# Performance work log

Hardware: AMD Instinct MI355X
Metric: run time of the kernel (lower is better)

## Reference

```python
import jax, jax.numpy as jnp
import numpy as np

N = 10000        # nodes
E = 320000       # edges (before self-loops)
G = 100          # graphs in batch
HEADS = 2
OUT = 125        # per-head out channels
NEG_SLOPE = 0.2  # PyG GATConv default leaky_relu slope


def setup_inputs() -> dict:
    key = jax.random.key(0)
    k = lambda i: jax.random.fold_in(key, i)
    rn = lambda i, shape, s=0.1: jax.random.normal(k(i), shape, jnp.float32) * s
    inp = {
        "x": jax.random.normal(k(0), (N, 336), jnp.float32),
        "edge_index": jax.random.randint(k(1), (2, E), 0, N, jnp.int32),
        "batch": jnp.sort(jax.random.randint(k(2), (N,), 0, G, jnp.int32)),
    }
    conv_in = [336, 250, 250, 250]
    for i, din in enumerate(conv_in, start=1):
        base = 10 * i
        inp[f"W{i}"] = rn(base, (din, HEADS * OUT))
        inp[f"asrc{i}"] = rn(base + 1, (HEADS, OUT))
        inp[f"adst{i}"] = rn(base + 2, (HEADS, OUT))
        inp[f"b{i}"] = jnp.zeros((HEADS * OUT,), jnp.float32)
    lin_dims = [(250, 200), (200, 100), (100, 100), (100, 29)]
    for i, (din, dout) in enumerate(lin_dims, start=1):
        inp[f"lw{i}"] = rn(100 + i, (din, dout))
        inp[f"lb{i}"] = jnp.zeros((dout,), jnp.float32)
    return inp


def gat_conv(x, src, dst, W, asrc, adst, b):
    # PyG GATConv (v1), concat heads, self-loops already in (src, dst).
    n = x.shape[0]
    h = (x @ W).reshape(n, HEADS, OUT)                    # [N,H,C]
    e_src = jnp.einsum('nhc,hc->nh', h, asrc)             # a_src . h_j
    e_dst = jnp.einsum('nhc,hc->nh', h, adst)             # a_dst . h_i
    e = jax.nn.leaky_relu(e_src[src] + e_dst[dst], NEG_SLOPE)  # [Etot,H]
    m = jax.ops.segment_max(e, dst, num_segments=n)       # segment softmax over incoming edges
    e = jnp.exp(e - m[dst])
    denom = jax.ops.segment_sum(e, dst, num_segments=n)
    alpha = e / (denom[dst] + 1e-16)                      # [Etot,H]
    out = jax.ops.segment_sum(alpha[:, :, None] * h[src], dst, num_segments=n)
    return out.reshape(n, HEADS * OUT) + b


def reference(x, edge_index, batch,
              W1, asrc1, adst1, b1, W2, asrc2, adst2, b2,
              W3, asrc3, adst3, b3, W4, asrc4, adst4, b4,
              lw1, lb1, lw2, lb2, lw3, lb3, lw4, lb4):
    n = x.shape[0]
    loop = jnp.arange(n, dtype=edge_index.dtype)
    src = jnp.concatenate([edge_index[0], loop])          # add_self_loops=True
    dst = jnp.concatenate([edge_index[1], loop])

    h = jax.nn.relu(gat_conv(x, src, dst, W1, asrc1, adst1, b1))
    h = jax.nn.relu(gat_conv(h, src, dst, W2, asrc2, adst2, b2))
    h = jax.nn.relu(gat_conv(h, src, dst, W3, asrc3, adst3, b3))
    h = jax.nn.relu(gat_conv(h, src, dst, W4, asrc4, adst4, b4))

    # global_mean_pool over graph ids
    sums = jax.ops.segment_sum(h, batch, num_segments=G)
    cnts = jax.ops.segment_sum(jnp.ones((n, 1), h.dtype), batch, num_segments=G)
    g = sums / jnp.maximum(cnts, 1.0)                     # [G,250]

    g = jax.nn.relu(g @ lw1 + lb1)
    g = jax.nn.relu(g @ lw2 + lb2)
    g = jax.nn.relu(g @ lw3 + lb3)
    return g @ lw4 + lb4                                  # [G,29]
```

## Files before the change

kernel.cpp:

```cpp
#include <hip/hip_runtime.h>
#include <hip/hip_bf16.h>

#define NNODES 10000
#define NEDGES 320000
#define ETOT   (NEDGES + NNODES)
#define NGRAPH 100
#define CH     250
#define HOUT   125
#define MPAD   10048
#define NTILE  157
#define KP0    352
#define KP1    256
#define HPAD   256
#define ECAP   128
#define DCAPW  128
#define APAD   264

typedef __attribute__((ext_vector_type(8))) short bf16x8;
typedef __attribute__((ext_vector_type(4))) float f32x4;

static __device__ __forceinline__ float bflo(unsigned int u){
  union{ unsigned int i; float f; } v; v.i = u << 16; return v.f;
}
static __device__ __forceinline__ float bfhi(unsigned int u){
  union{ unsigned int i; float f; } v; v.i = u & 0xffff0000u; return v.f;
}
static __device__ __forceinline__ unsigned short f2bfbits(float f){
  __hip_bfloat16 b = __float2bfloat16(f);
  union{ __hip_bfloat16 b; unsigned short s; } v; v.b = b; return v.s;
}

struct Args {
  const float* x; const int* eidx; const int* batch;
  const float *W0,*W1,*W2,*W3;
  __hip_bfloat16 *Abf0, *Wt0, *Wt1, *Wt2, *Wt3;
  int *cursor; unsigned short* bucket; int *gstart;
};

__global__ void k_pre(Args a){
  int gtid = blockIdx.x * blockDim.x + threadIdx.x;
  int gstr = gridDim.x * blockDim.x;
  for (int e = gtid; e < ETOT; e += gstr){
    int dst, src;
    if (e < NEDGES){ src = a.eidx[e]; dst = a.eidx[NEDGES + e]; }
    else           { src = e - NEDGES; dst = src; }
    int pos = atomicAdd(&a.cursor[dst], 1);
    if (pos < ECAP) a.bucket[(size_t)dst * ECAP + pos] = (unsigned short)src;
  }
  for (int n = gtid; n < NNODES; n += gstr){
    int b1 = a.batch[n];
    int b0 = (n == 0) ? -1 : a.batch[n-1];
    for (int b = b0 + 1; b <= b1; ++b) a.gstart[b] = n;
    if (n == NNODES - 1){
      for (int b = b1 + 1; b <= NGRAPH; ++b) a.gstart[b] = NNODES;
    }
  }
  for (int j = gtid; j < NNODES * 84; j += gstr){
    int r = j / 84, c4 = (j - r * 84) * 4;
    float4 v = *(const float4*)(a.x + (size_t)r * 336 + c4);
    ushort4 o;
    o.x = f2bfbits(v.x); o.y = f2bfbits(v.y); o.z = f2bfbits(v.z); o.w = f2bfbits(v.w);
    *(ushort4*)(a.Abf0 + (size_t)r * KP0 + c4) = o;
  }
  const int T0 = 16 * KP0 * 16;
  const int T1 = 16 * KP1 * 16;
  int tot = T0 + 3*T1;
  for (int i = gtid; i < tot; i += gstr){
    const float* W; __hip_bfloat16* Wt; int K, Kp, li;
    if (i < T0)             { W = a.W0; Wt = a.Wt0; K = 336; Kp = KP0; li = i; }
    else if (i < T0 +   T1) { W = a.W1; Wt = a.Wt1; K = CH;  Kp = KP1; li = i - T0; }
    else if (i < T0 + 2*T1) { W = a.W2; Wt = a.Wt2; K = CH;  Kp = KP1; li = i - T0 - T1; }
    else                    { W = a.W3; Wt = a.Wt3; K = CH;  Kp = KP1; li = i - T0 - 2*T1; }
    int KC = Kp >> 5;
    int nt = li / (Kp * 16);
    int rem = li % (Kp * 16);
    int k = rem / 16;
    int n = rem % 16;
    int col = nt * 16 + n;
    float v = (k < K && col < CH) ? W[(size_t)k * CH + col] : 0.f;
    Wt[(((size_t)nt * KC + (k >> 5)) * 16 + n) * 32 + (k & 31)] = __float2bfloat16(v);
  }
}

__global__ __launch_bounds__(256) void k_gemm(
    const __hip_bfloat16* __restrict__ A, const __hip_bfloat16* __restrict__ Wt,
    __hip_bfloat16* __restrict__ Cb, const float* __restrict__ asrc,
    const float* __restrict__ adst, float* __restrict__ esrc, float* __restrict__ edst,
    int Kp){
  int wv = threadIdx.x >> 6, lane = threadIdx.x & 63;
  int n16 = lane & 15, q = lane >> 4;
  int KC = Kp >> 5;
  int rowbase = blockIdx.x * 64 + wv * 16;
  int bn = blockIdx.y * 64;
  int nt0 = bn >> 4;
  const __hip_bfloat16* ap = A  + (size_t)(rowbase + n16) * Kp + q * 8;
  const __hip_bfloat16* bp = Wt + ((size_t)nt0 * KC * 16 + n16) * 32 + q * 8;
  f32x4 ac0 = {0.f,0.f,0.f,0.f}, ac1 = ac0, ac2 = ac0, ac3 = ac0;
  for (int kc = 0; kc < KC; ++kc){
    bf16x8 a  = *(const bf16x8*)(ap + (size_t)kc * 32);
    bf16x8 b0 = *(const bf16x8*)(bp + ((size_t)0 * KC + kc) * 512);
    bf16x8 b1 = *(const bf16x8*)(bp + ((size_t)1 * KC + kc) * 512);
    bf16x8 b2 = *(const bf16x8*)(bp + ((size_t)2 * KC + kc) * 512);
    bf16x8 b3 = *(const bf16x8*)(bp + ((size_t)3 * KC + kc) * 512);
    ac0 = __builtin_amdgcn_mfma_f32_16x16x32_bf16(a, b0, ac0, 0, 0, 0);
    ac1 = __builtin_amdgcn_mfma_f32_16x16x32_bf16(a, b1, ac1, 0, 0, 0);
    ac2 = __builtin_amdgcn_mfma_f32_16x16x32_bf16(a, b2, ac2, 0, 0, 0);
    ac3 = __builtin_amdgcn_mfma_f32_16x16x32_bf16(a, b3, ac3, 0, 0, 0);
  }
  float es0[4] = {}, es1[4] = {}, ed0a[4] = {}, ed1a[4] = {};
  #define SCORE_T(AC, T) { \
    int col = bn + (T)*16 + n16; \
    bool ok = col < CH; \
    float av = ok ? asrc[col] : 0.f; \
    float dv = ok ? adst[col] : 0.f; \
    bool hh = col >= HOUT; \
    float av0 = hh ? 0.f : av, av1 = hh ? av : 0.f; \
    float dv0 = hh ? 0.f : dv, dv1 = hh ? dv : 0.f; \
    _Pragma("unroll") \
    for (int r = 0; r < 4; ++r){ \
      es0[r] += AC[r]*av0; es1[r] += AC[r]*av1; \
      ed0a[r] += AC[r]*dv0; ed1a[r] += AC[r]*dv1; } }
  SCORE_T(ac0, 0) SCORE_T(ac1, 1) SCORE_T(ac2, 2) SCORE_T(ac3, 3)
  #undef SCORE_T
  #pragma unroll
  for (int off = 1; off < 16; off <<= 1){
    #pragma unroll
    for (int r = 0; r < 4; ++r){
      es0[r]  += __shfl_xor(es0[r],  off);
      es1[r]  += __shfl_xor(es1[r],  off);
      ed0a[r] += __shfl_xor(ed0a[r], off);
      ed1a[r] += __shfl_xor(ed1a[r], off);
    }
  }
  if (n16 == 0){
    #pragma unroll
    for (int r = 0; r < 4; ++r){
      int row = rowbase + q*4 + r;
      if (row < NNODES){
        atomicAdd(&esrc[row*2+0], es0[r]);
        atomicAdd(&esrc[row*2+1], es1[r]);
        atomicAdd(&edst[row*2+0], ed0a[r]);
        atomicAdd(&edst[row*2+1], ed1a[r]);
      }
    }
  }
  #pragma unroll
  for (int r = 0; r < 4; ++r){
    int row = rowbase + q * 4 + r;
    if (row >= NNODES) continue;
    int col = bn + n16;
    __hip_bfloat16* cb = Cb + (size_t)row * HPAD + col;
    cb[0]  = __float2bfloat16(col      < CH ? ac0[r] : 0.f);
    cb[16] = __float2bfloat16(col + 16 < CH ? ac1[r] : 0.f);
    cb[32] = __float2bfloat16(col + 32 < CH ? ac2[r] : 0.f);
    cb[48] = __float2bfloat16(col + 48 < CH ? ac3[r] : 0.f);
  }
}

#define GATHER8(SS, SX) \
  for (int it = half; it < deg; it += 16){ \
    uint4 dv[8]; float a0v[8], a1v[8]; \
    _Pragma("unroll") \
    for (int u = 0; u < 8; ++u){ \
      int ii = it + 2*u; \
      bool vld = ii < deg; \
      int jj = vld ? ii : 0; \
      int s = SS[jj]; \
      float2 xv = SX[jj]; \
      a0v[u] = vld ? xv.x : 0.f; \
      a1v[u] = vld ? xv.y : 0.f; \
      dv[u] = *(const uint4*)(hrow + (size_t)s * HPAD); \
    } \
    _Pragma("unroll") \
    for (int u = 0; u < 8; ++u){ \
      float a0 = a0v[u], a1 = a1v[u]; \
      acc[0] += (0 < n0 ? a0 : a1) * bflo(dv[u].x); \
      acc[1] += (1 < n0 ? a0 : a1) * bfhi(dv[u].x); \
      acc[2] += (2 < n0 ? a0 : a1) * bflo(dv[u].y); \
      acc[3] += (3 < n0 ? a0 : a1) * bfhi(dv[u].y); \
      acc[4] += (4 < n0 ? a0 : a1) * bflo(dv[u].z); \
      acc[5] += (5 < n0 ? a0 : a1) * bfhi(dv[u].z); \
      acc[6] += (6 < n0 ? a0 : a1) * bflo(dv[u].w); \
      acc[7] += (7 < n0 ? a0 : a1) * bfhi(dv[u].w); \
    } \
  }

__global__ __launch_bounds__(1024, 4) void k_fused(
    const __hip_bfloat16* __restrict__ hcur,
    const float* __restrict__ esrc, const float* __restrict__ edst,
    const int* __restrict__ degv, const unsigned short* __restrict__ bucket,
    const float* __restrict__ bias,
    const __hip_bfloat16* __restrict__ Wt,
    const float* __restrict__ asrc, const float* __restrict__ adst,
    __hip_bfloat16* __restrict__ hnext,
    float* __restrict__ esN, float* __restrict__ edN){
  int w = threadIdx.x >> 6, lane = threadIdx.x & 63;
  int nodebase = blockIdx.x * 16;
  int node = nodebase + w;
  __shared__ unsigned short s_src[16][DCAPW];
  __shared__ float2 s_x[16][DCAPW];
  __shared__ short  h_lds[16][APAD];
  __shared__ float  esp[16][16][2];
  __shared__ float  edp[16][16][2];
  int deg = degv[node]; if (deg > ECAP) deg = ECAP;
  const unsigned short* __restrict__ eb = bucket + (size_t)node * ECAP;
  float ed0 = edst[node*2+0], ed1 = edst[node*2+1];
  float sm0 = 0.f, sm1 = 0.f;
  for (int i = lane; i < deg; i += 64){
    int src = eb[i];
    float2 ev = *(const float2*)(esrc + (size_t)src * 2);
    float e0 = ev.x + ed0; e0 = e0 > 0.f ? e0 : 0.2f*e0;
    float e1 = ev.y + ed1; e1 = e1 > 0.f ? e1 : 0.2f*e1;
    float x0 = __expf(e0), x1 = __expf(e1);
    s_src[w][i] = (unsigned short)src; s_x[w][i] = make_float2(x0, x1);
    sm0 += x0; sm1 += x1;
  }
  #pragma unroll
  for (int off = 32; off > 0; off >>= 1){
    sm0 += __shfl_xor(sm0, off);
    sm1 += __shfl_xor(sm1, off);
  }
  float inv0 = 1.f / (sm0 + 1e-16f);
  float inv1 = 1.f / (sm1 + 1e-16f);
  int half = lane >> 5, hl = lane & 31;
  int c0 = hl * 8;
  int n0 = HOUT - c0; n0 = n0 < 0 ? 0 : (n0 > 8 ? 8 : n0);
  const __hip_bfloat16* __restrict__ hrow = hcur + c0;
  float acc[8] = {0.f,0.f,0.f,0.f,0.f,0.f,0.f,0.f};
  GATHER8(s_src[w], s_x[w])
  #pragma unroll
  for (int j = 0; j < 8; ++j) acc[j] += __shfl_xor(acc[j], 32);
  if (half == 0){
    if (hl < 31){
      float4 bA = *(const float4*)&bias[c0];
      float4 bB = *(const float4*)&bias[c0 + 4];
      float v0 = acc[0]*(0 < n0 ? inv0 : inv1) + bA.x;
      float v1 = acc[1]*(1 < n0 ? inv0 : inv1) + bA.y;
      float v2 = acc[2]*(2 < n0 ? inv0 : inv1) + bA.z;
      float v3 = acc[3]*(3 < n0 ? inv0 : inv1) + bA.w;
      float v4 = acc[4]*(4 < n0 ? inv0 : inv1) + bB.x;
      float v5 = acc[5]*(5 < n0 ? inv0 : inv1) + bB.y;
      float v6 = acc[6]*(6 < n0 ? inv0 : inv1) + bB.z;
      float v7 = acc[7]*(7 < n0 ? inv0 : inv1) + bB.w;
      v0 = v0 > 0.f ? v0 : 0.f; v1 = v1 > 0.f ? v1 : 0.f;
      v2 = v2 > 0.f ? v2 : 0.f; v3 = v3 > 0.f ? v3 : 0.f;
      v4 = v4 > 0.f ? v4 : 0.f; v5 = v5 > 0.f ? v5 : 0.f;
      v6 = v6 > 0.f ? v6 : 0.f; v7 = v7 > 0.f ? v7 : 0.f;
      uint4 o;
      o.x = (unsigned int)f2bfbits(v0) | ((unsigned int)f2bfbits(v1) << 16);
      o.y = (unsigned int)f2bfbits(v2) | ((unsigned int)f2bfbits(v3) << 16);
      o.z = (unsigned int)f2bfbits(v4) | ((unsigned int)f2bfbits(v5) << 16);
      o.w = (unsigned int)f2bfbits(v6) | ((unsigned int)f2bfbits(v7) << 16);
      *(uint4*)&h_lds[w][hl*8] = o;
    } else {
      float v0 = acc[0]*inv1 + bias[248];
      float v1 = acc[1]*inv1 + bias[249];
      v0 = v0 > 0.f ? v0 : 0.f; v1 = v1 > 0.f ? v1 : 0.f;
      uint4 o;
      o.x = (unsigned int)f2bfbits(v0) | ((unsigned int)f2bfbits(v1) << 16);
      o.y = 0u; o.z = 0u; o.w = 0u;
      *(uint4*)&h_lds[w][248] = o;
    }
  }
  __syncthreads();
  int n16 = lane & 15, q = lane >> 4;
  const int KC = KP1 >> 5;
  const __hip_bfloat16* bp = Wt + ((size_t)w * KC * 16 + n16) * 32 + q * 8;
  const short* ap = &h_lds[n16][q * 8];
  f32x4 ac = {0.f,0.f,0.f,0.f};
  #pragma unroll
  for (int kc = 0; kc < KC; ++kc){
    bf16x8 av = *(const bf16x8*)(ap + kc * 32);
    bf16x8 bv = *(const bf16x8*)(bp + (size_t)kc * 512);
    ac = __builtin_amdgcn_mfma_f32_16x16x32_bf16(av, bv, ac, 0, 0, 0);
  }
  int col = w * 16 + n16;
  bool ok = col < CH;
  float av_ = ok ? asrc[col] : 0.f;
  float dv_ = ok ? adst[col] : 0.f;
  bool hh = col >= HOUT;
  float av0 = hh ? 0.f : av_, av1 = hh ? av_ : 0.f;
  float dv0 = hh ? 0.f : dv_, dv1 = hh ? dv_ : 0.f;
  float es0[4], es1[4], edd0[4], edd1[4];
  #pragma unroll
  for (int r = 0; r < 4; ++r){
    es0[r] = ac[r]*av0; es1[r] = ac[r]*av1;
    edd0[r] = ac[r]*dv0; edd1[r] = ac[r]*dv1;
  }
  #pragma unroll
  for (int off = 1; off < 16; off <<= 1){
    #pragma unroll
    for (int r = 0; r < 4; ++r){
      es0[r]  += __shfl_xor(es0[r],  off);
      es1[r]  += __shfl_xor(es1[r],  off);
      edd0[r] += __shfl_xor(edd0[r], off);
      edd1[r] += __shfl_xor(edd1[r], off);
    }
  }
  if (n16 == 0){
    #pragma unroll
    for (int r = 0; r < 4; ++r){
      esp[w][q*4+r][0] = es0[r];  esp[w][q*4+r][1] = es1[r];
      edp[w][q*4+r][0] = edd0[r]; edp[w][q*4+r][1] = edd1[r];
    }
  }
  #pragma unroll
  for (int r = 0; r < 4; ++r){
    int row = nodebase + q*4 + r;
    hnext[(size_t)row * HPAD + col] = __float2bfloat16(ok ? ac[r] : 0.f);
  }
  __syncthreads();
  int t = threadIdx.x;
  if (t < 64){
    int row = t >> 2;
    int he = t & 1;
    int which = (t >> 1) & 1;
    float s = 0.f;
    #pragma unroll
    for (int w2 = 0; w2 < 16; ++w2)
      s += which ? edp[w2][row][he] : esp[w2][row][he];
    (which ? edN : esN)[(size_t)(nodebase + row) * 2 + he] = s;
  }
}

__global__ __launch_bounds__(256, 4) void k_attn(const __hip_bfloat16* __restrict__ h,
                        const float* __restrict__ esrc, const float* __restrict__ edst,
                        const int* __restrict__ degv, const unsigned short* __restrict__ bucket,
                        const float* __restrict__ bias, __hip_bfloat16* __restrict__ outb){
  int wv = threadIdx.x >> 6, lane = threadIdx.x & 63;
  int node = blockIdx.x * 4 + wv;
  __shared__ unsigned short s_src[4][DCAPW];
  __shared__ float2 s_x[4][DCAPW];
  int deg = degv[node]; if (deg > ECAP) deg = ECAP;
  const unsigned short* __restrict__ eb = bucket + (size_t)node * ECAP;
  float ed0 = edst[node*2+0], ed1 = edst[node*2+1];
  float sm0 = 0.f, sm1 = 0.f;
  for (int i = lane; i < deg; i += 64){
    int src = eb[i];
    float2 ev = *(const float2*)(esrc + (size_t)src * 2);
    float e0 = ev.x + ed0; e0 = e0 > 0.f ? e0 : 0.2f*e0;
    float e1 = ev.y + ed1; e1 = e1 > 0.f ? e1 : 0.2f*e1;
    float x0 = __expf(e0), x1 = __expf(e1);
    s_src[wv][i] = (unsigned short)src; s_x[wv][i] = make_float2(x0, x1);
    sm0 += x0; sm1 += x1;
  }
  #pragma unroll
  for (int off = 32; off > 0; off >>= 1){
    sm0 += __shfl_xor(sm0, off);
    sm1 += __shfl_xor(sm1, off);
  }
  float inv0 = 1.f / (sm0 + 1e-16f);
  float inv1 = 1.f / (sm1 + 1e-16f);
  int half = lane >> 5, hl = lane & 31;
  int c0 = hl * 8;
  int n0 = HOUT - c0; n0 = n0 < 0 ? 0 : (n0 > 8 ? 8 : n0);
  const __hip_bfloat16* __restrict__ hrow = h + c0;
  float acc[8] = {0.f,0.f,0.f,0.f,0.f,0.f,0.f,0.f};
  GATHER8(s_src[wv], s_x[wv])
  #pragma unroll
  for (int j = 0; j < 8; ++j) acc[j] += __shfl_xor(acc[j], 32);
  if (half == 0){
    if (hl < 31){
      float4 bA = *(const float4*)&bias[c0];
      float4 bB = *(const float4*)&bias[c0 + 4];
      float v0 = acc[0]*(0 < n0 ? inv0 : inv1) + bA.x;
      float v1 = acc[1]*(1 < n0 ? inv0 : inv1) + bA.y;
      float v2 = acc[2]*(2 < n0 ? inv0 : inv1) + bA.z;
      float v3 = acc[3]*(3 < n0 ? inv0 : inv1) + bA.w;
      float v4 = acc[4]*(4 < n0 ? inv0 : inv1) + bB.x;
      float v5 = acc[5]*(5 < n0 ? inv0 : inv1) + bB.y;
      float v6 = acc[6]*(6 < n0 ? inv0 : inv1) + bB.z;
      float v7 = acc[7]*(7 < n0 ? inv0 : inv1) + bB.w;
      v0 = v0 > 0.f ? v0 : 0.f; v1 = v1 > 0.f ? v1 : 0.f;
      v2 = v2 > 0.f ? v2 : 0.f; v3 = v3 > 0.f ? v3 : 0.f;
      v4 = v4 > 0.f ? v4 : 0.f; v5 = v5 > 0.f ? v5 : 0.f;
      v6 = v6 > 0.f ? v6 : 0.f; v7 = v7 > 0.f ? v7 : 0.f;
      uint4 o;
      o.x = (unsigned int)f2bfbits(v0) | ((unsigned int)f2bfbits(v1) << 16);
      o.y = (unsigned int)f2bfbits(v2) | ((unsigned int)f2bfbits(v3) << 16);
      o.z = (unsigned int)f2bfbits(v4) | ((unsigned int)f2bfbits(v5) << 16);
      o.w = (unsigned int)f2bfbits(v6) | ((unsigned int)f2bfbits(v7) << 16);
      *(uint4*)(outb + (size_t)node * KP1 + c0) = o;
    } else {
      float v0 = acc[0]*inv1 + bias[248];
      float v1 = acc[1]*inv1 + bias[249];
      v0 = v0 > 0.f ? v0 : 0.f; v1 = v1 > 0.f ? v1 : 0.f;
      unsigned int o = (unsigned int)f2bfbits(v0) | ((unsigned int)f2bfbits(v1) << 16);
      *(unsigned int*)(outb + (size_t)node * KP1 + 248) = o;
    }
  }
}

__global__ __launch_bounds__(256) void k_head(const __hip_bfloat16* __restrict__ xb,
                        const int* __restrict__ gstart,
                        const float* __restrict__ lw1, const float* __restrict__ lb1,
                        const float* __restrict__ lw2, const float* __restrict__ lb2,
                        const float* __restrict__ lw3, const float* __restrict__ lb3,
                        const float* __restrict__ lw4, const float* __restrict__ lb4,
                        float* __restrict__ out){
  int g = blockIdx.x;
  int tid = threadIdx.x;
  int s = gstart[g], e = gstart[g+1];
  __shared__ float gvec[256];
  __shared__ float m1[200];
  __shared__ float m2[112];
  __shared__ float m3[112];
  if (tid < 128){
    int c2 = tid * 2;
    const __hip_bfloat16* xp = xb + c2;
    float a0=0.f,a1=0.f,b0=0.f,b1=0.f;
    int n = s;
    for (; n + 3 < e; n += 4){
      unsigned int u0 = *(const unsigned int*)(xp + (size_t)n     * KP1);
      unsigned int u1 = *(const unsigned int*)(xp + (size_t)(n+1) * KP1);
      unsigned int u2 = *(const unsigned int*)(xp + (size_t)(n+2) * KP1);
      unsigned int u3 = *(const unsigned int*)(xp + (size_t)(n+3) * KP1);
      a0 += bflo(u0) + bflo(u2); a1 += bfhi(u0) + bfhi(u2);
      b0 += bflo(u1) + bflo(u3); b1 += bfhi(u1) + bfhi(u3);
    }
    for (; n < e; ++n){
      unsigned int u0 = *(const unsigned int*)(xp + (size_t)n * KP1);
      a0 += bflo(u0); a1 += bfhi(u0);
    }
    float scale = 1.f / fmaxf((float)(e - s), 1.f);
    gvec[c2]     = (a0 + b0) * scale;
    gvec[c2 + 1] = (a1 + b1) * scale;
  }
  __syncthreads();
  if (tid < 200){
    float a0=0.f,a1=0.f,a2=0.f,a3=0.f;
    int k = 0;
    for (; k + 3 < CH; k += 4){
      a0 += gvec[k]   * lw1[(size_t)k     * 200 + tid];
      a1 += gvec[k+1] * lw1[(size_t)(k+1) * 200 + tid];
      a2 += gvec[k+2] * lw1[(size_t)(k+2) * 200 + tid];
      a3 += gvec[k+3] * lw1[(size_t)(k+3) * 200 + tid];
    }
    for (; k < CH; ++k) a0 += gvec[k] * lw1[(size_t)k * 200 + tid];
    float v = a0 + a1 + a2 + a3 + lb1[tid];
    m1[tid] = v > 0.f ? v : 0.f;
  }
  __syncthreads();
  if (tid < 100){
    float a0=0.f,a1=0.f,a2=0.f,a3=0.f;
    for (int k = 0; k + 3 < 200; k += 4){
      a0 += m1[k]   * lw2[(size_t)k     * 100 + tid];
      a1 += m1[k+1] * lw2[(size_t)(k+1) * 100 + tid];
      a2 += m1[k+2] * lw2[(size_t)(k+2) * 100 + tid];
      a3 += m1[k+3] * lw2[(size_t)(k+3) * 100 + tid];
    }
    float v = a0 + a1 + a2 + a3 + lb2[tid];
    m2[tid] = v > 0.f ? v : 0.f;
  }
  __syncthreads();
  if (tid < 100){
    float a0=0.f,a1=0.f,a2=0.f,a3=0.f;
    for (int k = 0; k + 3 < 100; k += 4){
      a0 += m2[k]   * lw3[(size_t)k     * 100 + tid];
      a1 += m2[k+1] * lw3[(size_t)(k+1) * 100 + tid];
      a2 += m2[k+2] * lw3[(size_t)(k+2) * 100 + tid];
      a3 += m2[k+3] * lw3[(size_t)(k+3) * 100 + tid];
    }
    float v = a0 + a1 + a2 + a3 + lb3[tid];
    m3[tid] = v > 0.f ? v : 0.f;
  }
  __syncthreads();
  if (tid < 29){
    float a0=0.f,a1=0.f,a2=0.f,a3=0.f;
    for (int k = 0; k + 3 < 100; k += 4){
      a0 += m3[k]   * lw4[(size_t)k     * 29 + tid];
      a1 += m3[k+1] * lw4[(size_t)(k+1) * 29 + tid];
      a2 += m3[k+2] * lw4[(size_t)(k+2) * 29 + tid];
      a3 += m3[k+3] * lw4[(size_t)(k+3) * 29 + tid];
    }
    out[(size_t)g * 29 + tid] = a0 + a1 + a2 + a3 + lb4[tid];
  }
}

extern "C" void kernel_launch(void* const* d_in, const int* in_sizes, int n_in,
                              void* d_out, int out_size, void* d_ws, size_t ws_size,
                              hipStream_t stream){
  char* ws = (char*)d_ws;
  size_t off = 0;
  auto alloc = [&](size_t bytes)->void*{
    void* p = ws + off;
    off = (off + bytes + 255) & ~(size_t)255;
    return p;
  };
  __hip_bfloat16* hb16A = (__hip_bfloat16*)alloc((size_t)NNODES * HPAD * 2);
  __hip_bfloat16* hb16B = (__hip_bfloat16*)alloc((size_t)NNODES * HPAD * 2);
  __hip_bfloat16* Abf0 = (__hip_bfloat16*)alloc((size_t)MPAD * KP0 * 2);
  __hip_bfloat16* Abf  = (__hip_bfloat16*)alloc((size_t)MPAD * KP1 * 2);
  __hip_bfloat16* Wt0  = (__hip_bfloat16*)alloc((size_t)16 * KP0 * 16 * 2);
  __hip_bfloat16* Wt1  = (__hip_bfloat16*)alloc((size_t)16 * KP1 * 16 * 2);
  __hip_bfloat16* Wt2  = (__hip_bfloat16*)alloc((size_t)16 * KP1 * 16 * 2);
  __hip_bfloat16* Wt3  = (__hip_bfloat16*)alloc((size_t)16 * KP1 * 16 * 2);
  size_t zbeg = off;
  int*   cursor = (int*)  alloc((size_t)NNODES * 4);
  float* esA  = (float*)alloc((size_t)NNODES * 2 * 4);
  float* edA  = (float*)alloc((size_t)NNODES * 2 * 4);
  size_t zend = off;
  float* esB  = (float*)alloc((size_t)NNODES * 2 * 4);
  float* edB  = (float*)alloc((size_t)NNODES * 2 * 4);
  unsigned short* bucket = (unsigned short*)alloc((size_t)NNODES * ECAP * 2);
  int*   gstart = (int*)alloc((size_t)(NGRAPH + 1) * 4);

  hipMemsetAsync(ws + zbeg, 0, zend - zbeg, stream);

  Args a;
  a.x = (const float*)d_in[0];
  a.eidx = (const int*)d_in[1];
  a.batch = (const int*)d_in[2];
  a.W0 = (const float*)d_in[3];  a.W1 = (const float*)d_in[7];
  a.W2 = (const float*)d_in[11]; a.W3 = (const float*)d_in[15];
  a.Abf0 = Abf0;
  a.Wt0 = Wt0; a.Wt1 = Wt1; a.Wt2 = Wt2; a.Wt3 = Wt3;
  a.cursor = cursor; a.bucket = bucket; a.gstart = gstart;

  k_pre<<<(ETOT + 255)/256, 256, 0, stream>>>(a);

  k_gemm<<<dim3(NTILE, 4), 256, 0, stream>>>(Abf0, Wt0, hb16A,
      (const float*)d_in[4], (const float*)d_in[5], esA, edA, KP0);

  k_fused<<<NNODES/16, 1024, 0, stream>>>(hb16A, esA, edA, cursor, bucket,
      (const float*)d_in[6],  Wt1, (const float*)d_in[8],  (const float*)d_in[9],
      hb16B, esB, edB);
  k_fused<<<NNODES/16, 1024, 0, stream>>>(hb16B, esB, edB, cursor, bucket,
      (const float*)d_in[10], Wt2, (const float*)d_in[12], (const float*)d_in[13],
      hb16A, esA, edA);
  k_fused<<<NNODES/16, 1024, 0, stream>>>(hb16A, esA, edA, cursor, bucket,
      (const float*)d_in[14], Wt3, (const float*)d_in[16], (const float*)d_in[17],
      hb16B, esB, edB);

  k_attn<<<NNODES/4, 256, 0, stream>>>(hb16B, esB, edB, cursor, bucket,
      (const float*)d_in[18], Abf);

  k_head<<<NGRAPH, 256, 0, stream>>>(Abf, gstart,
      (const float*)d_in[19], (const float*)d_in[20],
      (const float*)d_in[21], (const float*)d_in[22],
      (const float*)d_in[23], (const float*)d_in[24],
      (const float*)d_in[25], (const float*)d_in[26],
      (float*)d_out);
}
```

Measured before the change: 310.9 us.

## Split fused gather+GEMM into separate column-sliced gather and GEMM kernels

Replaces the fused per-layer kernel (edge gather/softmax aggregation followed by an in-block MFMA GEMM) with two kernels: a gather kernel that splits each node's 256 output columns across 8 blocks of 32 columns, and a standalone GEMM kernel reading the aggregated activations from global memory. The aim is much more parallelism and better latency hiding in the gather, which was limited by one wave per node inside large 1024-thread blocks. The trade-off is that each column slice recomputes the per-node softmax weights (8x redundant exp work and esrc reads), plus an extra global round trip of the aggregated activations and extra kernel launches.

```diff
diff --git a/kernel.cpp b/kernel.cpp
--- a/kernel.cpp
+++ b/kernel.cpp
@@ -14,7 +14,6 @@
 #define HPAD   256
 #define ECAP   128
 #define DCAPW  128
-#define APAD   264
 
 typedef __attribute__((ext_vector_type(8))) short bf16x8;
 typedef __attribute__((ext_vector_type(4))) float f32x4;
@@ -157,178 +156,14 @@
   }
 }
 
-#define GATHER8(SS, SX) \
-  for (int it = half; it < deg; it += 16){ \
-    uint4 dv[8]; float a0v[8], a1v[8]; \
-    _Pragma("unroll") \
-    for (int u = 0; u < 8; ++u){ \
-      int ii = it + 2*u; \
-      bool vld = ii < deg; \
-      int jj = vld ? ii : 0; \
-      int s = SS[jj]; \
-      float2 xv = SX[jj]; \
-      a0v[u] = vld ? xv.x : 0.f; \
-      a1v[u] = vld ? xv.y : 0.f; \
-      dv[u] = *(const uint4*)(hrow + (size_t)s * HPAD); \
-    } \
-    _Pragma("unroll") \
-    for (int u = 0; u < 8; ++u){ \
-      float a0 = a0v[u], a1 = a1v[u]; \
-      acc[0] += (0 < n0 ? a0 : a1) * bflo(dv[u].x); \
-      acc[1] += (1 < n0 ? a0 : a1) * bfhi(dv[u].x); \
-      acc[2] += (2 < n0 ? a0 : a1) * bflo(dv[u].y); \
-      acc[3] += (3 < n0 ? a0 : a1) * bfhi(dv[u].y); \
-      acc[4] += (4 < n0 ? a0 : a1) * bflo(dv[u].z); \
-      acc[5] += (5 < n0 ? a0 : a1) * bfhi(dv[u].z); \
-      acc[6] += (6 < n0 ? a0 : a1) * bflo(dv[u].w); \
-      acc[7] += (7 < n0 ? a0 : a1) * bfhi(dv[u].w); \
-    } \
-  }
-
-__global__ __launch_bounds__(1024, 4) void k_fused(
-    const __hip_bfloat16* __restrict__ hcur,
+__global__ __launch_bounds__(256, 8) void k_gather(
+    const __hip_bfloat16* __restrict__ h,
     const float* __restrict__ esrc, const float* __restrict__ edst,
     const int* __restrict__ degv, const unsigned short* __restrict__ bucket,
-    const float* __restrict__ bias,
-    const __hip_bfloat16* __restrict__ Wt,
-    const float* __restrict__ asrc, const float* __restrict__ adst,
-    __hip_bfloat16* __restrict__ hnext,
-    float* __restrict__ esN, float* __restrict__ edN){
-  int w = threadIdx.x >> 6, lane = threadIdx.x & 63;
-  int nodebase = blockIdx.x * 16;
-  int node = nodebase + w;
-  __shared__ unsigned short s_src[16][DCAPW];
-  __shared__ float2 s_x[16][DCAPW];
-  __shared__ short  h_lds[16][APAD];
-  __shared__ float  esp[16][16][2];
-  __shared__ float  edp[16][16][2];
-  int deg = degv[node]; if (deg > ECAP) deg = ECAP;
-  const unsigned short* __restrict__ eb = bucket + (size_t)node * ECAP;
-  float ed0 = edst[node*2+0], ed1 = edst[node*2+1];
-  float sm0 = 0.f, sm1 = 0.f;
-  for (int i = lane; i < deg; i += 64){
-    int src = eb[i];
-    float2 ev = *(const float2*)(esrc + (size_t)src * 2);
-    float e0 = ev.x + ed0; e0 = e0 > 0.f ? e0 : 0.2f*e0;
-    float e1 = ev.y + ed1; e1 = e1 > 0.f ? e1 : 0.2f*e1;
-    float x0 = __expf(e0), x1 = __expf(e1);
-    s_src[w][i] = (unsigned short)src; s_x[w][i] = make_float2(x0, x1);
-    sm0 += x0; sm1 += x1;
-  }
-  #pragma unroll
-  for (int off = 32; off > 0; off >>= 1){
-    sm0 += __shfl_xor(sm0, off);
-    sm1 += __shfl_xor(sm1, off);
-  }
-  float inv0 = 1.f / (sm0 + 1e-16f);
-  float inv1 = 1.f / (sm1 + 1e-16f);
-  int half = lane >> 5, hl = lane & 31;
-  int c0 = hl * 8;
-  int n0 = HOUT - c0; n0 = n0 < 0 ? 0 : (n0 > 8 ? 8 : n0);
-  const __hip_bfloat16* __restrict__ hrow = hcur + c0;
-  float acc[8] = {0.f,0.f,0.f,0.f,0.f,0.f,0.f,0.f};
-  GATHER8(s_src[w], s_x[w])
-  #pragma unroll
-  for (int j = 0; j < 8; ++j) acc[j] += __shfl_xor(acc[j], 32);
-  if (half == 0){
-    if (hl < 31){
-      float4 bA = *(const float4*)&bias[c0];
-      float4 bB = *(const float4*)&bias[c0 + 4];
-      float v0 = acc[0]*(0 < n0 ? inv0 : inv1) + bA.x;
-      float v1 = acc[1]*(1 < n0 ? inv0 : inv1) + bA.y;
-      float v2 = acc[2]*(2 < n0 ? inv0 : inv1) + bA.z;
-      float v3 = acc[3]*(3 < n0 ? inv0 : inv1) + bA.w;
-      float v4 = acc[4]*(4 < n0 ? inv0 : inv1) + bB.x;
-      float v5 = acc[5]*(5 < n0 ? inv0 : inv1) + bB.y;
-      float v6 = acc[6]*(6 < n0 ? inv0 : inv1) + bB.z;
-      float v7 = acc[7]*(7 < n0 ? inv0 : inv1) + bB.w;
-      v0 = v0 > 0.f ? v0 : 0.f; v1 = v1 > 0.f ? v1 : 0.f;
-      v2 = v2 > 0.f ? v2 : 0.f; v3 = v3 > 0.f ? v3 : 0.f;
-      v4 = v4 > 0.f ? v4 : 0.f; v5 = v5 > 0.f ? v5 : 0.f;
-      v6 = v6 > 0.f ? v6 : 0.f; v7 = v7 > 0.f ? v7 : 0.f;
-      uint4 o;
-      o.x = (unsigned int)f2bfbits(v0) | ((unsigned int)f2bfbits(v1) << 16);
-      o.y = (unsigned int)f2bfbits(v2) | ((unsigned int)f2bfbits(v3) << 16);
-      o.z = (unsigned int)f2bfbits(v4) | ((unsigned int)f2bfbits(v5) << 16);
-      o.w = (unsigned int)f2bfbits(v6) | ((unsigned int)f2bfbits(v7) << 16);
-      *(uint4*)&h_lds[w][hl*8] = o;
-    } else {
-      float v0 = acc[0]*inv1 + bias[248];
-      float v1 = acc[1]*inv1 + bias[249];
-      v0 = v0 > 0.f ? v0 : 0.f; v1 = v1 > 0.f ? v1 : 0.f;
-      uint4 o;
-      o.x = (unsigned int)f2bfbits(v0) | ((unsigned int)f2bfbits(v1) << 16);
-      o.y = 0u; o.z = 0u; o.w = 0u;
-      *(uint4*)&h_lds[w][248] = o;
-    }
-  }
-  __syncthreads();
-  int n16 = lane & 15, q = lane >> 4;
-  const int KC = KP1 >> 5;
-  const __hip_bfloat16* bp = Wt + ((size_t)w * KC * 16 + n16) * 32 + q * 8;
-  const short* ap = &h_lds[n16][q * 8];
-  f32x4 ac = {0.f,0.f,0.f,0.f};
-  #pragma unroll
-  for (int kc = 0; kc < KC; ++kc){
-    bf16x8 av = *(const bf16x8*)(ap + kc * 32);
-    bf16x8 bv = *(const bf16x8*)(bp + (size_t)kc * 512);
-    ac = __builtin_amdgcn_mfma_f32_16x16x32_bf16(av, bv, ac, 0, 0, 0);
-  }
-  int col = w * 16 + n16;
-  bool ok = col < CH;
-  float av_ = ok ? asrc[col] : 0.f;
-  float dv_ = ok ? adst[col] : 0.f;
-  bool hh = col >= HOUT;
-  float av0 = hh ? 0.f : av_, av1 = hh ? av_ : 0.f;
-  float dv0 = hh ? 0.f : dv_, dv1 = hh ? dv_ : 0.f;
-  float es0[4], es1[4], edd0[4], edd1[4];
-  #pragma unroll
-  for (int r = 0; r < 4; ++r){
-    es0[r] = ac[r]*av0; es1[r] = ac[r]*av1;
-    edd0[r] = ac[r]*dv0; edd1[r] = ac[r]*dv1;
-  }
-  #pragma unroll
-  for (int off = 1; off < 16; off <<= 1){
-    #pragma unroll
-    for (int r = 0; r < 4; ++r){
-      es0[r]  += __shfl_xor(es0[r],  off);
-      es1[r]  += __shfl_xor(es1[r],  off);
-      edd0[r] += __shfl_xor(edd0[r], off);
-      edd1[r] += __shfl_xor(edd1[r], off);
-    }
-  }
-  if (n16 == 0){
-    #pragma unroll
-    for (int r = 0; r < 4; ++r){
-      esp[w][q*4+r][0] = es0[r];  esp[w][q*4+r][1] = es1[r];
-      edp[w][q*4+r][0] = edd0[r]; edp[w][q*4+r][1] = edd1[r];
-    }
-  }
-  #pragma unroll
-  for (int r = 0; r < 4; ++r){
-    int row = nodebase + q*4 + r;
-    hnext[(size_t)row * HPAD + col] = __float2bfloat16(ok ? ac[r] : 0.f);
-  }
-  __syncthreads();
-  int t = threadIdx.x;
-  if (t < 64){
-    int row = t >> 2;
-    int he = t & 1;
-    int which = (t >> 1) & 1;
-    float s = 0.f;
-    #pragma unroll
-    for (int w2 = 0; w2 < 16; ++w2)
-      s += which ? edp[w2][row][he] : esp[w2][row][he];
-    (which ? edN : esN)[(size_t)(nodebase + row) * 2 + he] = s;
-  }
-}
-
-__global__ __launch_bounds__(256, 4) void k_attn(const __hip_bfloat16* __restrict__ h,
-                        const float* __restrict__ esrc, const float* __restrict__ edst,
-                        const int* __restrict__ degv, const unsigned short* __restrict__ bucket,
-                        const float* __restrict__ bias, __hip_bfloat16* __restrict__ outb){
+    const float* __restrict__ bias, __hip_bfloat16* __restrict__ outb){
   int wv = threadIdx.x >> 6, lane = threadIdx.x & 63;
-  int node = blockIdx.x * 4 + wv;
+  int s = blockIdx.x & 7;
+  int node = (blockIdx.x >> 3) * 4 + wv;
   __shared__ unsigned short s_src[4][DCAPW];
   __shared__ float2 s_x[4][DCAPW];
   int deg = degv[node]; if (deg > ECAP) deg = ECAP;
@@ -351,43 +186,114 @@
   }
   float inv0 = 1.f / (sm0 + 1e-16f);
   float inv1 = 1.f / (sm1 + 1e-16f);
-  int half = lane >> 5, hl = lane & 31;
-  int c0 = hl * 8;
-  int n0 = HOUT - c0; n0 = n0 < 0 ? 0 : (n0 > 8 ? 8 : n0);
-  const __hip_bfloat16* __restrict__ hrow = h + c0;
-  float acc[8] = {0.f,0.f,0.f,0.f,0.f,0.f,0.f,0.f};
-  GATHER8(s_src[wv], s_x[wv])
-  #pragma unroll
-  for (int j = 0; j < 8; ++j) acc[j] += __shfl_xor(acc[j], 32);
-  if (half == 0){
-    if (hl < 31){
-      float4 bA = *(const float4*)&bias[c0];
-      float4 bB = *(const float4*)&bias[c0 + 4];
-      float v0 = acc[0]*(0 < n0 ? inv0 : inv1) + bA.x;
-      float v1 = acc[1]*(1 < n0 ? inv0 : inv1) + bA.y;
-      float v2 = acc[2]*(2 < n0 ? inv0 : inv1) + bA.z;
-      float v3 = acc[3]*(3 < n0 ? inv0 : inv1) + bA.w;
-      float v4 = acc[4]*(4 < n0 ? inv0 : inv1) + bB.x;
-      float v5 = acc[5]*(5 < n0 ? inv0 : inv1) + bB.y;
-      float v6 = acc[6]*(6 < n0 ? inv0 : inv1) + bB.z;
-      float v7 = acc[7]*(7 < n0 ? inv0 : inv1) + bB.w;
-      v0 = v0 > 0.f ? v0 : 0.f; v1 = v1 > 0.f ? v1 : 0.f;
-      v2 = v2 > 0.f ? v2 : 0.f; v3 = v3 > 0.f ? v3 : 0.f;
-      v4 = v4 > 0.f ? v4 : 0.f; v5 = v5 > 0.f ? v5 : 0.f;
-      v6 = v6 > 0.f ? v6 : 0.f; v7 = v7 > 0.f ? v7 : 0.f;
-      uint4 o;
-      o.x = (unsigned int)f2bfbits(v0) | ((unsigned int)f2bfbits(v1) << 16);
-      o.y = (unsigned int)f2bfbits(v2) | ((unsigned int)f2bfbits(v3) << 16);
-      o.z = (unsigned int)f2bfbits(v4) | ((unsigned int)f2bfbits(v5) << 16);
-      o.w = (unsigned int)f2bfbits(v6) | ((unsigned int)f2bfbits(v7) << 16);
-      *(uint4*)(outb + (size_t)node * KP1 + c0) = o;
-    } else {
-      float v0 = acc[0]*inv1 + bias[248];
-      float v1 = acc[1]*inv1 + bias[249];
-      v0 = v0 > 0.f ? v0 : 0.f; v1 = v1 > 0.f ? v1 : 0.f;
-      unsigned int o = (unsigned int)f2bfbits(v0) | ((unsigned int)f2bfbits(v1) << 16);
-      *(unsigned int*)(outb + (size_t)node * KP1 + 248) = o;
-    }
+  int quarter = lane >> 4, ql = lane & 15;
+  int cL = s * 32 + ql * 2;
+  bool selL = cL < HOUT, selH = (cL + 1) < HOUT;
+  const __hip_bfloat16* __restrict__ hq = h + cL;
+  float accL = 0.f, accH = 0.f;
+  for (int it = quarter; it < deg; it += 16){
+    unsigned int dv[4]; float aL[4], aH[4];
+    #pragma unroll
+    for (int u = 0; u < 4; ++u){
+      int ii = it + 4*u;
+      bool vld = ii < deg;
+      int jj = vld ? ii : 0;
+      int sr = s_src[wv][jj];
+      float2 xv = s_x[wv][jj];
+      float x0 = vld ? xv.x : 0.f, x1 = vld ? xv.y : 0.f;
+      aL[u] = selL ? x0 : x1;
+      aH[u] = selH ? x0 : x1;
+      dv[u] = *(const unsigned int*)(hq + (size_t)sr * HPAD);
+    }
+    #pragma unroll
+    for (int u = 0; u < 4; ++u){
+      accL += aL[u] * bflo(dv[u]);
+      accH += aH[u] * bfhi(dv[u]);
+    }
+  }
+  accL += __shfl_xor(accL, 16); accL += __shfl_xor(accL, 32);
+  accH += __shfl_xor(accH, 16); accH += __shfl_xor(accH, 32);
+  if (lane < 16){
+    float vL = 0.f, vH = 0.f;
+    if (cL < CH){
+      vL = accL * (selL ? inv0 : inv1) + bias[cL];
+      vL = vL > 0.f ? vL : 0.f;
+    }
+    if (cL + 1 < CH){
+      vH = accH * (selH ? inv0 : inv1) + bias[cL + 1];
+      vH = vH > 0.f ? vH : 0.f;
+    }
+    *(unsigned int*)(outb + (size_t)node * HPAD + cL) =
+        (unsigned int)f2bfbits(vL) | ((unsigned int)f2bfbits(vH) << 16);
+  }
+}
+
+__global__ __launch_bounds__(1024, 8) void k_gemm2(
+    const __hip_bfloat16* __restrict__ A, const __hip_bfloat16* __restrict__ Wt,
+    const float* __restrict__ asrc, const float* __restrict__ adst,
+    __hip_bfloat16* __restrict__ hnext,
+    float* __restrict__ esN, float* __restrict__ edN){
+  int w = threadIdx.x >> 6, lane = threadIdx.x & 63;
+  int nodebase = blockIdx.x * 16;
+  __shared__ float esp[16][16][2];
+  __shared__ float edp[16][16][2];
+  int n16 = lane & 15, q = lane >> 4;
+  const int KC = KP1 >> 5;
+  const __hip_bfloat16* bp = Wt + ((size_t)w * KC * 16 + n16) * 32 + q * 8;
+  const __hip_bfloat16* ap = A + (size_t)(nodebase + n16) * KP1 + q * 8;
+  f32x4 ac = {0.f,0.f,0.f,0.f};
+  #pragma unroll
+  for (int kc = 0; kc < KC; ++kc){
+    bf16x8 av = *(const bf16x8*)(ap + (size_t)kc * 32);
+    bf16x8 bv = *(const bf16x8*)(bp + (size_t)kc * 512);
+    ac = __builtin_amdgcn_mfma_f32_16x16x32_bf16(av, bv, ac, 0, 0, 0);
+  }
+  int col = w * 16 + n16;
+  bool ok = col < CH;
+  float av_ = ok ? asrc[col] : 0.f;
+  float dv_ = ok ? adst[col] : 0.f;
+  bool hh = col >= HOUT;
+  float av0 = hh ? 0.f : av_, av1 = hh ? av_ : 0.f;
+  float dv0 = hh ? 0.f : dv_, dv1 = hh ? dv_ : 0.f;
+  float es0[4], es1[4], edd0[4], edd1[4];
+  #pragma unroll
+  for (int r = 0; r < 4; ++r){
+    es0[r] = ac[r]*av0; es1[r] = ac[r]*av1;
+    edd0[r] = ac[r]*dv0; edd1[r] = ac[r]*dv1;
+  }
+  #pragma unroll
+  for (int off = 1; off < 16; off <<= 1){
+    #pragma unroll
+    for (int r = 0; r < 4; ++r){
+      es0[r]  += __shfl_xor(es0[r],  off);
+      es1[r]  += __shfl_xor(es1[r],  off);
+      edd0[r] += __shfl_xor(edd0[r], off);
+      edd1[r] += __shfl_xor(edd1[r], off);
+    }
+  }
+  if (n16 == 0){
+    #pragma unroll
+    for (int r = 0; r < 4; ++r){
+      esp[w][q*4+r][0] = es0[r];  esp[w][q*4+r][1] = es1[r];
+      edp[w][q*4+r][0] = edd0[r]; edp[w][q*4+r][1] = edd1[r];
+    }
+  }
+  #pragma unroll
+  for (int r = 0; r < 4; ++r){
+    int row = nodebase + q*4 + r;
+    hnext[(size_t)row * HPAD + col] = __float2bfloat16(ok ? ac[r] : 0.f);
+  }
+  __syncthreads();
+  int t = threadIdx.x;
+  if (t < 64){
+    int row = t >> 2;
+    int he = t & 1;
+    int which = (t >> 1) & 1;
+    float sum = 0.f;
+    #pragma unroll
+    for (int w2 = 0; w2 < 16; ++w2)
+      sum += which ? edp[w2][row][he] : esp[w2][row][he];
+    (which ? edN : esN)[(size_t)(nodebase + row) * 2 + he] = sum;
   }
 }
 
@@ -522,17 +428,21 @@
   k_gemm<<<dim3(NTILE, 4), 256, 0, stream>>>(Abf0, Wt0, hb16A,
       (const float*)d_in[4], (const float*)d_in[5], esA, edA, KP0);
 
-  k_fused<<<NNODES/16, 1024, 0, stream>>>(hb16A, esA, edA, cursor, bucket,
-      (const float*)d_in[6],  Wt1, (const float*)d_in[8],  (const float*)d_in[9],
-      hb16B, esB, edB);
-  k_fused<<<NNODES/16, 1024, 0, stream>>>(hb16B, esB, edB, cursor, bucket,
-      (const float*)d_in[10], Wt2, (const float*)d_in[12], (const float*)d_in[13],
-      hb16A, esA, edA);
-  k_fused<<<NNODES/16, 1024, 0, stream>>>(hb16A, esA, edA, cursor, bucket,
-      (const float*)d_in[14], Wt3, (const float*)d_in[16], (const float*)d_in[17],
-      hb16B, esB, edB);
-
-  k_attn<<<NNODES/4, 256, 0, stream>>>(hb16B, esB, edB, cursor, bucket,
+  const int GG = (NNODES/4) * 8;
+
+  k_gather<<<GG, 256, 0, stream>>>(hb16A, esA, edA, cursor, bucket,
+      (const float*)d_in[6], Abf);
+  k_gemm2<<<NNODES/16, 1024, 0, stream>>>(Abf, Wt1,
+      (const float*)d_in[8], (const float*)d_in[9], hb16B, esB, edB);
+  k_gather<<<GG, 256, 0, stream>>>(hb16B, esB, edB, cursor, bucket,
+      (const float*)d_in[10], Abf);
+  k_gemm2<<<NNODES/16, 1024, 0, stream>>>(Abf, Wt2,
+      (const float*)d_in[12], (const float*)d_in[13], hb16A, esA, edA);
+  k_gather<<<GG, 256, 0, stream>>>(hb16A, esA, edA, cursor, bucket,
+      (const float*)d_in[14], Abf);
+  k_gemm2<<<NNODES/16, 1024, 0, stream>>>(Abf, Wt3,
+      (const float*)d_in[16], (const float*)d_in[17], hb16B, esB, edB);
+  k_gather<<<GG, 256, 0, stream>>>(hb16B, esB, edB, cursor, bucket,
       (const float*)d_in[18], Abf);
 
   k_head<<<NGRAPH, 256, 0, stream>>>(Abf, gstart,
```

Measured after the change: 398.2 us. 28.1% more time.
